# Optimization experiments

Measured on AMD Instinct MI355X. Metric: run time of the kernel, lower is better.

The kernel has to match this reference:

```python
import jax, jax.numpy as jnp
import numpy as np

N_NODES = 100000
N_EDGES = 1200000
N_GRAPHS = 512
IN_DIM, HID, N_CLS = 16, 64, 2
EPS = 1e-5


def setup_inputs() -> dict:
    key = jax.random.key(0)
    ks = jax.random.split(key, 24)
    d = {}
    d["x"] = jax.random.normal(ks[0], (N_NODES, IN_DIM), dtype=jnp.float32)
    d["edge_index"] = jax.random.randint(ks[1], (2, N_EDGES), 0, N_NODES, dtype=jnp.int32)
    d["batch_ids"] = jnp.sort(jax.random.randint(ks[2], (N_NODES,), 0, N_GRAPHS, dtype=jnp.int32))
    # input batchnorm affine
    d["bn_in_g"] = jnp.ones((IN_DIM,), jnp.float32)
    d["bn_in_b"] = jnp.zeros((IN_DIM,), jnp.float32)
    # 3 GCN layers: weight, bias, bn gamma, bn beta
    dims = [(IN_DIM, HID), (HID, HID), (HID, HID)]
    for i, (ci, co) in enumerate(dims):
        s = 1.0 / np.sqrt(ci)
        d[f"W{i}"] = jax.random.uniform(ks[3 + 4 * i], (ci, co), jnp.float32, -s, s)
        d[f"b{i}"] = jnp.zeros((co,), jnp.float32)
        d[f"g{i}"] = jnp.ones((co,), jnp.float32)
        d[f"be{i}"] = jnp.zeros((co,), jnp.float32)
    # classifier head: Linear(HID,HID) -> ReLU -> Linear(HID,N_CLS)
    s = 1.0 / np.sqrt(HID)
    d["Wc1"] = jax.random.uniform(ks[20], (HID, HID), jnp.float32, -s, s)
    d["bc1"] = jax.random.uniform(ks[21], (HID,), jnp.float32, -s, s)
    d["Wc2"] = jax.random.uniform(ks[22], (HID, N_CLS), jnp.float32, -s, s)
    d["bc2"] = jax.random.uniform(ks[23], (N_CLS,), jnp.float32, -s, s)
    return d


def _batchnorm(x, g, b):
    # training-mode BatchNorm1d: biased batch stats over nodes
    m = jnp.mean(x, axis=0)
    v = jnp.mean(jnp.square(x - m), axis=0)
    return (x - m) * jax.lax.rsqrt(v + EPS) * g + b


def _gcn(x, W, b, src, dst, dis):
    # GCNConv: out[i] = sum_{j->i} dis[j]*dis[i] * (x_j W) + b  (self-loops included in src/dst)
    h = x @ W                                  # [N, co]
    msg = h[src] * (dis[src] * dis[dst])[:, None]  # [E+N, co] gather
    return jax.ops.segment_sum(msg, dst, num_segments=N_NODES) + b


def reference(x, bn_in_g, bn_in_b, W0, b0, g0, be0, W1, b1, g1, be1,
              W2, b2, g2, be2, Wc1, bc1, Wc2, bc2, edge_index, batch_ids):
    loops = jnp.arange(N_NODES, dtype=edge_index.dtype)
    src = jnp.concatenate([edge_index[0], loops])
    dst = jnp.concatenate([edge_index[1], loops])
    deg = jax.ops.segment_sum(jnp.ones(src.shape[0], x.dtype), dst, num_segments=N_NODES)
    dis = jnp.where(deg > 0, jax.lax.rsqrt(jnp.maximum(deg, 1e-12)), 0.0)

    h = _batchnorm(x, bn_in_g, bn_in_b)
    for W, b, g, be in ((W0, b0, g0, be0), (W1, b1, g1, be1), (W2, b2, g2, be2)):
        h = jax.nn.relu(_batchnorm(_gcn(h, W, b, src, dst, dis), g, be))

    # global mean pool over graphs
    sums = jax.ops.segment_sum(h, batch_ids, num_segments=N_GRAPHS)
    cnt = jax.ops.segment_sum(jnp.ones((N_NODES,), h.dtype), batch_ids, num_segments=N_GRAPHS)
    pooled = sums / jnp.maximum(cnt, 1.0)[:, None]

    # classifier head (dropout omitted: eval mode)
    z = jax.nn.relu(pooled @ Wc1 + bc1)
    return z @ Wc2 + bc2
```

## Files before the change

kernel.cpp:

```cpp
#include <hip/hip_runtime.h>
#include <hip/hip_bf16.h>

#define N_NODES 100000
#define N_EDGES 1200000
#define N_GRAPHS 512
#define HID 64
#define IN_DIM 16
#define EPS 1e-5f

#define NB_BUCKETS 391
#define BUCKET_SPAN 256
#define REGION 4096
#define BIN_TILE 4096
#define CSR_LEN (N_EDGES + N_NODES)
#define NREP 64


__global__ void bin_kernel(const int* __restrict__ ei, int* __restrict__ bucketCnt,
                           int* __restrict__ regions) {
    __shared__ int hist[NB_BUCKETS], basem[NB_BUCKETS], cur[NB_BUCKETS];
    int t = threadIdx.x;
    for (int i = t; i < NB_BUCKETS; i += 256) { hist[i] = 0; cur[i] = 0; }
    __syncthreads();
    int e0 = blockIdx.x * BIN_TILE;
    int srcs[16], dsts[16];
#pragma unroll
    for (int i = 0; i < 16; i++) {
        int e = e0 + t + i * 256;
        if (e < N_EDGES) {
            srcs[i] = ei[e];
            dsts[i] = ei[N_EDGES + e];
            atomicAdd(&hist[dsts[i] >> 8], 1);
        } else {
            dsts[i] = -1;
        }
    }
    __syncthreads();
    for (int i = t; i < NB_BUCKETS; i += 256) {
        int h = hist[i];
        basem[i] = h ? atomicAdd(&bucketCnt[i], h) : 0;
    }
    __syncthreads();
#pragma unroll
    for (int i = 0; i < 16; i++) {
        if (dsts[i] >= 0) {
            int b = dsts[i] >> 8;
            int pos = basem[b] + atomicAdd(&cur[b], 1);
            if (pos < REGION)
                regions[b * REGION + pos] = srcs[i] | ((dsts[i] & 255) << 17);
        }
    }
}

__global__ void build_kernel(const int* __restrict__ regions, const int* __restrict__ bucketCnt,
                             int* __restrict__ csrOff, int* __restrict__ csrSrc,
                             float* __restrict__ dis) {
    __shared__ int deg[256], off[256], cur[256];
    __shared__ int slice[REGION + 256];
    __shared__ int sTot, sBase;
    int b = blockIdx.x, t = threadIdx.x;
    {
        int s = 0;
        for (int i = t; i < NB_BUCKETS; i += 256)
            if (i < b) s += min(bucketCnt[i], REGION);
        deg[t] = s;
        __syncthreads();
        for (int k = 128; k > 0; k >>= 1) {
            if (t < k) deg[t] += deg[t + k];
            __syncthreads();
        }
        if (t == 0) sBase = deg[0] + b * BUCKET_SPAN;
        __syncthreads();
    }
    int bb = sBase;
    int cnt = min(bucketCnt[b], REGION);
    int nbase = b * BUCKET_SPAN;
    int n = nbase + t;
    bool valid = (n < N_NODES);
    deg[t] = valid ? 1 : 0;
    __syncthreads();
    for (int i = t; i < cnt; i += 256) {
        int rec = regions[b * REGION + i];
        atomicAdd(&deg[rec >> 17], 1);
    }
    __syncthreads();
    int d = deg[t];
    off[t] = d;
    __syncthreads();
    for (int s = 1; s < 256; s <<= 1) {
        int v = (t >= s) ? off[t - s] : 0;
        __syncthreads();
        off[t] += v;
        __syncthreads();
    }
    int excl = off[t] - d;
    if (valid) {
        csrOff[n] = bb + excl;
        dis[n] = rsqrtf((float)d);
    }
    if (b == 0 && t == 0) csrOff[N_NODES] = CSR_LEN;
    if (t == 255) sTot = off[255];
    cur[t] = excl;
    __syncthreads();
    if (valid) {
        int pos = atomicAdd(&cur[t], 1);
        slice[pos] = n;
    }
    for (int i = t; i < cnt; i += 256) {
        int rec = regions[b * REGION + i];
        int pos = atomicAdd(&cur[rec >> 17], 1);
        slice[pos] = rec & 0x1FFFF;
    }
    __syncthreads();
    int tot = sTot;
    for (int i = t; i < tot; i += 256) csrSrc[bb + i] = slice[i];
}


__global__ void stats_x(const float* __restrict__ x, float* __restrict__ sums,
                        float* __restrict__ sumsq, float* __restrict__ hwBuf) {
    __shared__ float ls[16], lq[16];
    int t = threadIdx.x;
    if (blockIdx.x == 0 && t < 16)
        ((float4*)(hwBuf + (size_t)N_NODES * HID))[t] = make_float4(0.f, 0.f, 0.f, 0.f);
    if (t < 16) { ls[t] = 0.f; lq[t] = 0.f; }
    __syncthreads();
    float s = 0.f, q = 0.f;
    const int total = N_NODES * IN_DIM;
    for (int i = blockIdx.x * blockDim.x + t; i < total; i += gridDim.x * blockDim.x) {
        float v = x[i];
        s += v; q += v * v;
    }
    int k = t & 15;
    atomicAdd(&ls[k], s);
    atomicAdd(&lq[k], q);
    __syncthreads();
    if (t < 16) { atomicAdd(&sums[t], ls[t]); atomicAdd(&sumsq[t], lq[t]); }
}

__device__ __forceinline__ void bn_coef(const float* sums, const float* sumsq,
                                        const float* gamma, const float* beta, int k,
                                        float& sc, float& sh) {
    const float invn = 1.0f / (float)N_NODES;
    float m = sums[k] * invn;
    float var = sumsq[k] * invn - m * m;
    float rs = rsqrtf(var + EPS);
    sc = gamma[k] * rs;
    sh = beta[k] - m * sc;
}

__global__ void reduce_stats(const float* __restrict__ rep, float* __restrict__ outStats) {
    int j = threadIdx.x;
    float s = 0.f;
    for (int r = 0; r < NREP; r++) s += rep[r * 128 + j];
    outStats[j] = s;
}


__global__ void premsg_kernel(const float* __restrict__ x, const float* __restrict__ sums,
                              const float* __restrict__ sumsq, const float* __restrict__ gamma,
                              const float* __restrict__ beta, const float* __restrict__ dis,
                              float4* __restrict__ m4) {
    __shared__ float sc16[16], sh16[16];
    int t = threadIdx.x;
    if (t < 16) bn_coef(sums, sumsq, gamma, beta, t, sc16[t], sh16[t]);
    __syncthreads();
    int idx = blockIdx.x * 256 + t;
    if (idx < (N_NODES + 1) * 4) {
        int n = idx >> 2, c = idx & 3;
        float4 v = make_float4(0.f, 0.f, 0.f, 0.f);
        if (n < N_NODES) {
            float4 h = ((const float4*)x)[idx];
            float d = dis[n];
            v.x = (h.x * sc16[c * 4 + 0] + sh16[c * 4 + 0]) * d;
            v.y = (h.y * sc16[c * 4 + 1] + sh16[c * 4 + 1]) * d;
            v.z = (h.z * sc16[c * 4 + 2] + sh16[c * 4 + 2]) * d;
            v.w = (h.w * sc16[c * 4 + 3] + sh16[c * 4 + 3]) * d;
        }
        m4[idx] = v;
    }
}

__global__ void agg16_gemm0_kernel(const float4* __restrict__ m4, const int* __restrict__ csrOff,
                                   const int* __restrict__ csrSrc, const float* __restrict__ dis,
                                   const float* __restrict__ W, const float* __restrict__ bias,
                                   float* __restrict__ y, float* __restrict__ statsRep) {
    __shared__ float Ws[IN_DIM][HID];
    int t = threadIdx.x;
    for (int i = t; i < IN_DIM * HID; i += 256) Ws[i >> 6][i & 63] = W[i];
    __syncthreads();
    const int lane = t & 63;
    const int wid = t >> 6;
    const int q = lane >> 2;
    const int fl = lane & 3;
    const int baseLane = lane & ~3;
    const int wave = blockIdx.x * 4 + wid;
    const int nwaves = gridDim.x * 4;
    float b = bias[lane];
    float sv = 0.f, qv = 0.f;

    for (int n = wave; n < N_NODES; n += nwaves) {
        int beg = csrOff[n], end = csrOff[n + 1];
        float4 acc = make_float4(0.f, 0.f, 0.f, 0.f);
        int e = beg + q;
        int i0 = (e < end) ? csrSrc[e] : N_NODES;
        int i1 = (e + 16 < end) ? csrSrc[e + 16] : N_NODES;
        while (e < end) {
            int j0 = i0, j1 = i1;
            e += 32;
            i0 = (e < end) ? csrSrc[e] : N_NODES;
            i1 = (e + 16 < end) ? csrSrc[e + 16] : N_NODES;
            float4 v0 = m4[(size_t)j0 * 4 + fl];
            float4 v1 = m4[(size_t)j1 * 4 + fl];
            acc.x += v0.x + v1.x; acc.y += v0.y + v1.y;
            acc.z += v0.z + v1.z; acc.w += v0.w + v1.w;
        }
#pragma unroll
        for (int m = 4; m <= 32; m <<= 1) {
            acc.x += __shfl_xor(acc.x, m, 64);
            acc.y += __shfl_xor(acc.y, m, 64);
            acc.z += __shfl_xor(acc.z, m, 64);
            acc.w += __shfl_xor(acc.w, m, 64);
        }
        float d = dis[n];
        acc.x *= d; acc.y *= d; acc.z *= d; acc.w *= d;
        float yv = b;
#pragma unroll
        for (int sf = 0; sf < 4; sf++) {
            float ax = __shfl(acc.x, baseLane + sf, 64);
            float ay = __shfl(acc.y, baseLane + sf, 64);
            float az = __shfl(acc.z, baseLane + sf, 64);
            float aw = __shfl(acc.w, baseLane + sf, 64);
            yv += ax * Ws[sf * 4 + 0][lane];
            yv += ay * Ws[sf * 4 + 1][lane];
            yv += az * Ws[sf * 4 + 2][lane];
            yv += aw * Ws[sf * 4 + 3][lane];
        }
        y[(size_t)n * HID + lane] = yv;
        sv += yv;
        qv += yv * yv;
    }
    __shared__ float ls[4][64], lq[4][64];
    ls[wid][lane] = sv;
    lq[wid][lane] = qv;
    __syncthreads();
    if (wid == 0) {
        float S = ls[0][lane] + ls[1][lane] + ls[2][lane] + ls[3][lane];
        float Q = lq[0][lane] + lq[1][lane] + lq[2][lane] + lq[3][lane];
        float* rep = statsRep + (blockIdx.x & (NREP - 1)) * 128;
        atomicAdd(&rep[lane], S);
        atomicAdd(&rep[64 + lane], Q);
    }
}


#define G64_ROWS 128
__global__ void gemm64_kernel(const float* __restrict__ hin, const float* __restrict__ W,
                              const float* __restrict__ sums, const float* __restrict__ sumsq,
                              const float* __restrict__ gamma, const float* __restrict__ beta,
                              const float* __restrict__ dis, float* __restrict__ hout) {
    __shared__ float Ws[HID * HID];
    __shared__ float hs[G64_ROWS][HID + 1];
    __shared__ float scb[64], shb[64];
    int t = threadIdx.x;
    int fg = t & 15;
    int rg = t >> 4;
    int base = blockIdx.x * G64_ROWS;

    if (t < 64) bn_coef(sums, sumsq, gamma, beta, t, scb[t], shb[t]);
    {
        const float4* W4 = (const float4*)W;
        float4* Ws4 = (float4*)Ws;
        for (int i = t; i < HID * HID / 4; i += 256) Ws4[i] = W4[i];
    }
    __syncthreads();
    {
        const float4* hin4 = (const float4*)hin;
        for (int i = t; i < G64_ROWS * 16; i += 256) {
            int r = i >> 4, c = i & 15;
            int n = base + r;
            float4 v = make_float4(0.f, 0.f, 0.f, 0.f);
            if (n < N_NODES) {
                float4 h = hin4[n * 16 + c];
                v.x = fmaxf(h.x * scb[c * 4 + 0] + shb[c * 4 + 0], 0.f);
                v.y = fmaxf(h.y * scb[c * 4 + 1] + shb[c * 4 + 1], 0.f);
                v.z = fmaxf(h.z * scb[c * 4 + 2] + shb[c * 4 + 2], 0.f);
                v.w = fmaxf(h.w * scb[c * 4 + 3] + shb[c * 4 + 3], 0.f);
            }
            hs[r][c * 4 + 0] = v.x;
            hs[r][c * 4 + 1] = v.y;
            hs[r][c * 4 + 2] = v.z;
            hs[r][c * 4 + 3] = v.w;
        }
    }
    __syncthreads();

    float4 acc[8];
#pragma unroll
    for (int r = 0; r < 8; r++) acc[r] = make_float4(0.f, 0.f, 0.f, 0.f);
    const float4* Ws4 = (const float4*)Ws;
    for (int k = 0; k < HID; k++) {
        float4 wk = Ws4[k * 16 + fg];
#pragma unroll
        for (int r = 0; r < 8; r++) {
            float h = hs[rg * 8 + r][k];
            acc[r].x += h * wk.x;
            acc[r].y += h * wk.y;
            acc[r].z += h * wk.z;
            acc[r].w += h * wk.w;
        }
    }
    float4* hout4 = (float4*)hout;
#pragma unroll
    for (int r = 0; r < 8; r++) {
        int n = base + rg * 8 + r;
        if (n < N_NODES) {
            float dsc = dis[n];
            float4 o = acc[r];
            o.x *= dsc; o.y *= dsc; o.z *= dsc; o.w *= dsc;
            hout4[n * 16 + fg] = o;
        }
    }
}


__global__ void aggregate_kernel(const float4* __restrict__ hw4, const int* __restrict__ csrOff,
                                 const int* __restrict__ csrSrc, const float* __restrict__ dis,
                                 const float* __restrict__ bias, float4* __restrict__ y4,
                                 float* __restrict__ statsRep) {
    const int lane = threadIdx.x & 63;
    const int wid = threadIdx.x >> 6;
    const int q = lane >> 4;
    const int fl = lane & 15;
    const int wave = blockIdx.x * 4 + wid;
    const int nwaves = gridDim.x * 4;

    const float4 bias4 = ((const float4*)bias)[fl];
    float4 s_acc = make_float4(0.f, 0.f, 0.f, 0.f);
    float4 q_acc = make_float4(0.f, 0.f, 0.f, 0.f);

    for (int n = wave; n < N_NODES; n += nwaves) {
        int beg = csrOff[n], end = csrOff[n + 1];
        float4 acc = make_float4(0.f, 0.f, 0.f, 0.f);
        int e = beg + q;
        int i0 = (e < end) ? csrSrc[e] : N_NODES;
        int i1 = (e + 4 < end) ? csrSrc[e + 4] : N_NODES;
        while (e < end) {
            int j0 = i0, j1 = i1;
            e += 8;
            i0 = (e < end) ? csrSrc[e] : N_NODES;
            i1 = (e + 4 < end) ? csrSrc[e + 4] : N_NODES;
            float4 v0 = hw4[(size_t)j0 * 16 + fl];
            float4 v1 = hw4[(size_t)j1 * 16 + fl];
            acc.x += v0.x + v1.x; acc.y += v0.y + v1.y;
            acc.z += v0.z + v1.z; acc.w += v0.w + v1.w;
        }
        acc.x += __shfl_xor(acc.x, 16, 64);
        acc.y += __shfl_xor(acc.y, 16, 64);
        acc.z += __shfl_xor(acc.z, 16, 64);
        acc.w += __shfl_xor(acc.w, 16, 64);
        acc.x += __shfl_xor(acc.x, 32, 64);
        acc.y += __shfl_xor(acc.y, 32, 64);
        acc.z += __shfl_xor(acc.z, 32, 64);
        acc.w += __shfl_xor(acc.w, 32, 64);
        if (q == 0) {
            float d = dis[n];
            float4 val;
            val.x = acc.x * d + bias4.x;
            val.y = acc.y * d + bias4.y;
            val.z = acc.z * d + bias4.z;
            val.w = acc.w * d + bias4.w;
            y4[(size_t)n * 16 + fl] = val;
            s_acc.x += val.x; s_acc.y += val.y; s_acc.z += val.z; s_acc.w += val.w;
            q_acc.x += val.x * val.x; q_acc.y += val.y * val.y;
            q_acc.z += val.z * val.z; q_acc.w += val.w * val.w;
        }
    }
    __shared__ float ls[4][64], lq[4][64];
    ls[wid][lane] = 0.f;
    lq[wid][lane] = 0.f;
    if (q == 0) {
        ls[wid][fl * 4 + 0] = s_acc.x; ls[wid][fl * 4 + 1] = s_acc.y;
        ls[wid][fl * 4 + 2] = s_acc.z; ls[wid][fl * 4 + 3] = s_acc.w;
        lq[wid][fl * 4 + 0] = q_acc.x; lq[wid][fl * 4 + 1] = q_acc.y;
        lq[wid][fl * 4 + 2] = q_acc.z; lq[wid][fl * 4 + 3] = q_acc.w;
    }
    __syncthreads();
    if (wid == 0) {
        float S = ls[0][lane] + ls[1][lane] + ls[2][lane] + ls[3][lane];
        float Q = lq[0][lane] + lq[1][lane] + lq[2][lane] + lq[3][lane];
        float* rep = statsRep + (blockIdx.x & (NREP - 1)) * 128;
        atomicAdd(&rep[lane], S);
        atomicAdd(&rep[64 + lane], Q);
    }
}


#define POOL_CHUNK 256
__global__ void pool_kernel(const float* __restrict__ y, const int* __restrict__ batch,
                            const float* __restrict__ sums, const float* __restrict__ sumsq,
                            const float* __restrict__ gamma, const float* __restrict__ beta,
                            float* __restrict__ pool, float* __restrict__ cnt) {
    int f = threadIdx.x & 63;
    int nl = threadIdx.x >> 6;
    float sc, sh;
    bn_coef(sums, sumsq, gamma, beta, f, sc, sh);
    int base = blockIdx.x * POOL_CHUNK;
    int endn = min(base + POOL_CHUNK, N_NODES);
    int g_cur = -1;
    float acc = 0.f;
    float c_acc = 0.f;
    for (int n = base + nl; n < endn; n += 4) {
        int g = batch[n];
        float v = fmaxf(y[n * HID + f] * sc + sh, 0.f);
        if (g != g_cur) {
            if (g_cur >= 0) {
                atomicAdd(&pool[g_cur * HID + f], acc);
                if (f == 0) atomicAdd(&cnt[g_cur], c_acc);
            }
            g_cur = g;
            acc = 0.f;
            c_acc = 0.f;
        }
        acc += v;
        c_acc += 1.f;
    }
    if (g_cur >= 0) {
        atomicAdd(&pool[g_cur * HID + f], acc);
        if (f == 0) atomicAdd(&cnt[g_cur], c_acc);
    }
}

__global__ void head_kernel(const float* __restrict__ pool, const float* __restrict__ cnt,
                            const float* __restrict__ Wc1, const float* __restrict__ bc1,
                            const float* __restrict__ Wc2, const float* __restrict__ bc2,
                            float* __restrict__ out) {
    int g = blockIdx.x;
    int f = threadIdx.x;
    __shared__ float p[64], z[64];
    float c = fmaxf(cnt[g], 1.0f);
    p[f] = pool[g * HID + f] / c;
    __syncthreads();
    float acc = bc1[f];
    for (int k = 0; k < 64; k++) acc += p[k] * Wc1[k * 64 + f];
    z[f] = fmaxf(acc, 0.f);
    __syncthreads();
    if (f < 2) {
        float o = bc2[f];
        for (int k = 0; k < 64; k++) o += z[k] * Wc2[k * 2 + f];
        out[g * 2 + f] = o;
    }
}


extern "C" void kernel_launch(void* const* d_in, const int* in_sizes, int n_in,
                              void* d_out, int out_size, void* d_ws, size_t ws_size,
                              hipStream_t stream) {
    const float* x      = (const float*)d_in[0];
    const int*   ei     = (const int*)d_in[1];
    const int*   batch  = (const int*)d_in[2];
    const float* bn_in_g = (const float*)d_in[3];
    const float* bn_in_b = (const float*)d_in[4];
    const float* W0 = (const float*)d_in[5];
    const float* b0 = (const float*)d_in[6];
    const float* g0 = (const float*)d_in[7];
    const float* be0 = (const float*)d_in[8];
    const float* W1 = (const float*)d_in[9];
    const float* b1 = (const float*)d_in[10];
    const float* g1 = (const float*)d_in[11];
    const float* be1 = (const float*)d_in[12];
    const float* W2 = (const float*)d_in[13];
    const float* b2 = (const float*)d_in[14];
    const float* g2 = (const float*)d_in[15];
    const float* be2 = (const float*)d_in[16];
    const float* Wc1 = (const float*)d_in[17];
    const float* bc1 = (const float*)d_in[18];
    const float* Wc2 = (const float*)d_in[19];
    const float* bc2 = (const float*)d_in[20];
    float* out = (float*)d_out;

    char* w = (char*)d_ws;
    size_t off = 0;
    auto take = [&](size_t bytes) {
        size_t r = off;
        off += (bytes + 255) & ~(size_t)255;
        return r;
    };
    float* stats    = (float*)(w + take(4 * 256 * 4));
    float* statsRep = (float*)(w + take(3 * NREP * 128 * 4));
    float* pool     = (float*)(w + take((size_t)N_GRAPHS * HID * 4));
    float* cnt      = (float*)(w + take((size_t)N_GRAPHS * 4));
    int* bucketCnt  = (int*)(w + take((size_t)NB_BUCKETS * 4));
    size_t zero_end = off;
    float* dis    = (float*)(w + take((size_t)N_NODES * 4));
    int* csrOff   = (int*)(w + take((size_t)(N_NODES + 1) * 4));
    int* csrSrc   = (int*)(w + take((size_t)(CSR_LEN + 64) * 4));
    float* hwBuf  = (float*)(w + take((size_t)(N_NODES + 1) * HID * 4));
    float* yBuf   = (float*)(w + take((size_t)N_NODES * HID * 4));
    int* regions  = (int*)hwBuf;
    float* msgBuf = (float*)hwBuf;
    (void)ws_size; (void)n_in; (void)in_sizes; (void)out_size;

    hipMemsetAsync(w, 0, zero_end, stream);

    const int nbBin  = (N_EDGES + BIN_TILE - 1) / BIN_TILE;
    const int nbPre  = ((N_NODES + 1) * 4 + 255) / 256;
    const int nbG64  = (N_NODES + G64_ROWS - 1) / G64_ROWS;
    const int nbAgg  = 4096;

    bin_kernel<<<nbBin, 256, 0, stream>>>(ei, bucketCnt, regions);
    build_kernel<<<NB_BUCKETS, 256, 0, stream>>>(regions, bucketCnt, csrOff, csrSrc, dis);

    float* s0 = stats + 0 * 256;
    float* s1 = stats + 1 * 256;
    float* s2 = stats + 2 * 256;
    float* s3 = stats + 3 * 256;
    float* rep1 = statsRep + 0 * NREP * 128;
    float* rep2 = statsRep + 1 * NREP * 128;
    float* rep3 = statsRep + 2 * NREP * 128;

    stats_x<<<256, 256, 0, stream>>>(x, s0, s0 + 64, hwBuf);

    premsg_kernel<<<nbPre, 256, 0, stream>>>(x, s0, s0 + 64, bn_in_g, bn_in_b, dis,
                                             (float4*)msgBuf);
    agg16_gemm0_kernel<<<nbAgg, 256, 0, stream>>>((const float4*)msgBuf, csrOff, csrSrc, dis,
                                                  W0, b0, yBuf, rep1);
    reduce_stats<<<1, 128, 0, stream>>>(rep1, s1);

    gemm64_kernel<<<nbG64, 256, 0, stream>>>(yBuf, W1, s1, s1 + 64, g0, be0, dis, hwBuf);
    aggregate_kernel<<<nbAgg, 256, 0, stream>>>((const float4*)hwBuf, csrOff, csrSrc, dis, b1,
                                                (float4*)yBuf, rep2);
    reduce_stats<<<1, 128, 0, stream>>>(rep2, s2);

    gemm64_kernel<<<nbG64, 256, 0, stream>>>(yBuf, W2, s2, s2 + 64, g1, be1, dis, hwBuf);
    aggregate_kernel<<<nbAgg, 256, 0, stream>>>((const float4*)hwBuf, csrOff, csrSrc, dis, b2,
                                                (float4*)yBuf, rep3);
    reduce_stats<<<1, 128, 0, stream>>>(rep3, s3);

    const int nbPool = (N_NODES + POOL_CHUNK - 1) / POOL_CHUNK;
    pool_kernel<<<nbPool, 256, 0, stream>>>(yBuf, batch, s3, s3 + 64, g2, be2, pool, cnt);
    head_kernel<<<N_GRAPHS, 64, 0, stream>>>(pool, cnt, Wc1, bc1, Wc2, bc2, out);
}
```

Before: 367.8 us.

## Store gathered message buffers in fp16 and widen aggregation lanes to half8

The pre-scaled message buffers that the aggregation kernels gather from are now stored as fp16 instead of fp32, which halves the bytes moved per random neighbor gather. The 64-wide aggregation is remapped so each lane loads a half8 (16 bytes), letting 8 edges be processed in parallel per wave instead of 4, with accumulation still done in fp32. The 16-dim message buffer gets its own allocation rather than aliasing hwBuf. The cost is reduced precision in the messages, which may perturb the batchnorm statistics and the final outputs.

```diff
diff --git a/kernel.cpp b/kernel.cpp
--- a/kernel.cpp
+++ b/kernel.cpp
@@ -14,6 +14,9 @@
 #define BIN_TILE 4096
 #define CSR_LEN (N_EDGES + N_NODES)
 #define NREP 64
+
+typedef _Float16 half4 __attribute__((ext_vector_type(4)));
+typedef _Float16 half8 __attribute__((ext_vector_type(8)));
 
 
 __global__ void bin_kernel(const int* __restrict__ ei, int* __restrict__ bucketCnt,
@@ -118,10 +121,10 @@
 
 
 __global__ void stats_x(const float* __restrict__ x, float* __restrict__ sums,
-                        float* __restrict__ sumsq, float* __restrict__ hwBuf) {
+                        float* __restrict__ sumsq, _Float16* __restrict__ hwBuf) {
     __shared__ float ls[16], lq[16];
     int t = threadIdx.x;
-    if (blockIdx.x == 0 && t < 16)
+    if (blockIdx.x == 0 && t < 8)
         ((float4*)(hwBuf + (size_t)N_NODES * HID))[t] = make_float4(0.f, 0.f, 0.f, 0.f);
     if (t < 16) { ls[t] = 0.f; lq[t] = 0.f; }
     __syncthreads();
@@ -160,7 +163,7 @@
 __global__ void premsg_kernel(const float* __restrict__ x, const float* __restrict__ sums,
                               const float* __restrict__ sumsq, const float* __restrict__ gamma,
                               const float* __restrict__ beta, const float* __restrict__ dis,
-                              float4* __restrict__ m4) {
+                              half4* __restrict__ m4) {
     __shared__ float sc16[16], sh16[16];
     int t = threadIdx.x;
     if (t < 16) bn_coef(sums, sumsq, gamma, beta, t, sc16[t], sh16[t]);
@@ -168,20 +171,21 @@
     int idx = blockIdx.x * 256 + t;
     if (idx < (N_NODES + 1) * 4) {
         int n = idx >> 2, c = idx & 3;
-        float4 v = make_float4(0.f, 0.f, 0.f, 0.f);
+        half4 o;
+        o.x = (_Float16)0.f; o.y = (_Float16)0.f; o.z = (_Float16)0.f; o.w = (_Float16)0.f;
         if (n < N_NODES) {
             float4 h = ((const float4*)x)[idx];
             float d = dis[n];
-            v.x = (h.x * sc16[c * 4 + 0] + sh16[c * 4 + 0]) * d;
-            v.y = (h.y * sc16[c * 4 + 1] + sh16[c * 4 + 1]) * d;
-            v.z = (h.z * sc16[c * 4 + 2] + sh16[c * 4 + 2]) * d;
-            v.w = (h.w * sc16[c * 4 + 3] + sh16[c * 4 + 3]) * d;
-        }
-        m4[idx] = v;
-    }
-}
-
-__global__ void agg16_gemm0_kernel(const float4* __restrict__ m4, const int* __restrict__ csrOff,
+            o.x = (_Float16)((h.x * sc16[c * 4 + 0] + sh16[c * 4 + 0]) * d);
+            o.y = (_Float16)((h.y * sc16[c * 4 + 1] + sh16[c * 4 + 1]) * d);
+            o.z = (_Float16)((h.z * sc16[c * 4 + 2] + sh16[c * 4 + 2]) * d);
+            o.w = (_Float16)((h.w * sc16[c * 4 + 3] + sh16[c * 4 + 3]) * d);
+        }
+        m4[idx] = o;
+    }
+}
+
+__global__ void agg16_gemm0_kernel(const half4* __restrict__ m4, const int* __restrict__ csrOff,
                                    const int* __restrict__ csrSrc, const float* __restrict__ dis,
                                    const float* __restrict__ W, const float* __restrict__ bias,
                                    float* __restrict__ y, float* __restrict__ statsRep) {
@@ -210,10 +214,12 @@
             e += 32;
             i0 = (e < end) ? csrSrc[e] : N_NODES;
             i1 = (e + 16 < end) ? csrSrc[e + 16] : N_NODES;
-            float4 v0 = m4[(size_t)j0 * 4 + fl];
-            float4 v1 = m4[(size_t)j1 * 4 + fl];
-            acc.x += v0.x + v1.x; acc.y += v0.y + v1.y;
-            acc.z += v0.z + v1.z; acc.w += v0.w + v1.w;
+            half4 v0 = m4[(size_t)j0 * 4 + fl];
+            half4 v1 = m4[(size_t)j1 * 4 + fl];
+            acc.x += (float)v0.x + (float)v1.x;
+            acc.y += (float)v0.y + (float)v1.y;
+            acc.z += (float)v0.z + (float)v1.z;
+            acc.w += (float)v0.w + (float)v1.w;
         }
 #pragma unroll
         for (int m = 4; m <= 32; m <<= 1) {
@@ -258,7 +264,7 @@
 __global__ void gemm64_kernel(const float* __restrict__ hin, const float* __restrict__ W,
                               const float* __restrict__ sums, const float* __restrict__ sumsq,
                               const float* __restrict__ gamma, const float* __restrict__ beta,
-                              const float* __restrict__ dis, float* __restrict__ hout) {
+                              const float* __restrict__ dis, _Float16* __restrict__ hout) {
     __shared__ float Ws[HID * HID];
     __shared__ float hs[G64_ROWS][HID + 1];
     __shared__ float scb[64], shb[64];
@@ -310,80 +316,83 @@
             acc[r].w += h * wk.w;
         }
     }
-    float4* hout4 = (float4*)hout;
+    half4* hout4 = (half4*)hout;
 #pragma unroll
     for (int r = 0; r < 8; r++) {
         int n = base + rg * 8 + r;
         if (n < N_NODES) {
             float dsc = dis[n];
-            float4 o = acc[r];
-            o.x *= dsc; o.y *= dsc; o.z *= dsc; o.w *= dsc;
+            half4 o;
+            o.x = (_Float16)(acc[r].x * dsc);
+            o.y = (_Float16)(acc[r].y * dsc);
+            o.z = (_Float16)(acc[r].z * dsc);
+            o.w = (_Float16)(acc[r].w * dsc);
             hout4[n * 16 + fg] = o;
         }
     }
 }
 
 
-__global__ void aggregate_kernel(const float4* __restrict__ hw4, const int* __restrict__ csrOff,
+__global__ void aggregate_kernel(const half8* __restrict__ hwh, const int* __restrict__ csrOff,
                                  const int* __restrict__ csrSrc, const float* __restrict__ dis,
                                  const float* __restrict__ bias, float4* __restrict__ y4,
                                  float* __restrict__ statsRep) {
     const int lane = threadIdx.x & 63;
     const int wid = threadIdx.x >> 6;
-    const int q = lane >> 4;
-    const int fl = lane & 15;
+    const int o = lane >> 3;
+    const int c = lane & 7;
     const int wave = blockIdx.x * 4 + wid;
     const int nwaves = gridDim.x * 4;
 
-    const float4 bias4 = ((const float4*)bias)[fl];
-    float4 s_acc = make_float4(0.f, 0.f, 0.f, 0.f);
-    float4 q_acc = make_float4(0.f, 0.f, 0.f, 0.f);
+    const float4 bv0 = ((const float4*)bias)[c * 2];
+    const float4 bv1 = ((const float4*)bias)[c * 2 + 1];
+    float sa[8], qa[8];
+#pragma unroll
+    for (int j = 0; j < 8; j++) { sa[j] = 0.f; qa[j] = 0.f; }
 
     for (int n = wave; n < N_NODES; n += nwaves) {
         int beg = csrOff[n], end = csrOff[n + 1];
-        float4 acc = make_float4(0.f, 0.f, 0.f, 0.f);
-        int e = beg + q;
+        float acc[8];
+#pragma unroll
+        for (int j = 0; j < 8; j++) acc[j] = 0.f;
+        int e = beg + o;
         int i0 = (e < end) ? csrSrc[e] : N_NODES;
-        int i1 = (e + 4 < end) ? csrSrc[e + 4] : N_NODES;
+        int i1 = (e + 8 < end) ? csrSrc[e + 8] : N_NODES;
         while (e < end) {
             int j0 = i0, j1 = i1;
-            e += 8;
+            e += 16;
             i0 = (e < end) ? csrSrc[e] : N_NODES;
-            i1 = (e + 4 < end) ? csrSrc[e + 4] : N_NODES;
-            float4 v0 = hw4[(size_t)j0 * 16 + fl];
-            float4 v1 = hw4[(size_t)j1 * 16 + fl];
-            acc.x += v0.x + v1.x; acc.y += v0.y + v1.y;
-            acc.z += v0.z + v1.z; acc.w += v0.w + v1.w;
-        }
-        acc.x += __shfl_xor(acc.x, 16, 64);
-        acc.y += __shfl_xor(acc.y, 16, 64);
-        acc.z += __shfl_xor(acc.z, 16, 64);
-        acc.w += __shfl_xor(acc.w, 16, 64);
-        acc.x += __shfl_xor(acc.x, 32, 64);
-        acc.y += __shfl_xor(acc.y, 32, 64);
-        acc.z += __shfl_xor(acc.z, 32, 64);
-        acc.w += __shfl_xor(acc.w, 32, 64);
-        if (q == 0) {
+            i1 = (e + 8 < end) ? csrSrc[e + 8] : N_NODES;
+            half8 h0 = hwh[(size_t)j0 * 8 + c];
+            half8 h1 = hwh[(size_t)j1 * 8 + c];
+#pragma unroll
+            for (int j = 0; j < 8; j++) acc[j] += (float)h0[j] + (float)h1[j];
+        }
+#pragma unroll
+        for (int j = 0; j < 8; j++) {
+            acc[j] += __shfl_xor(acc[j], 8, 64);
+            acc[j] += __shfl_xor(acc[j], 16, 64);
+            acc[j] += __shfl_xor(acc[j], 32, 64);
+        }
+        if (o == 0) {
             float d = dis[n];
-            float4 val;
-            val.x = acc.x * d + bias4.x;
-            val.y = acc.y * d + bias4.y;
-            val.z = acc.z * d + bias4.z;
-            val.w = acc.w * d + bias4.w;
-            y4[(size_t)n * 16 + fl] = val;
-            s_acc.x += val.x; s_acc.y += val.y; s_acc.z += val.z; s_acc.w += val.w;
-            q_acc.x += val.x * val.x; q_acc.y += val.y * val.y;
-            q_acc.z += val.z * val.z; q_acc.w += val.w * val.w;
+            float val[8];
+            val[0] = acc[0] * d + bv0.x; val[1] = acc[1] * d + bv0.y;
+            val[2] = acc[2] * d + bv0.z; val[3] = acc[3] * d + bv0.w;
+            val[4] = acc[4] * d + bv1.x; val[5] = acc[5] * d + bv1.y;
+            val[6] = acc[6] * d + bv1.z; val[7] = acc[7] * d + bv1.w;
+            y4[(size_t)n * 16 + c * 2] = make_float4(val[0], val[1], val[2], val[3]);
+            y4[(size_t)n * 16 + c * 2 + 1] = make_float4(val[4], val[5], val[6], val[7]);
+#pragma unroll
+            for (int j = 0; j < 8; j++) { sa[j] += val[j]; qa[j] += val[j] * val[j]; }
         }
     }
     __shared__ float ls[4][64], lq[4][64];
     ls[wid][lane] = 0.f;
     lq[wid][lane] = 0.f;
-    if (q == 0) {
-        ls[wid][fl * 4 + 0] = s_acc.x; ls[wid][fl * 4 + 1] = s_acc.y;
-        ls[wid][fl * 4 + 2] = s_acc.z; ls[wid][fl * 4 + 3] = s_acc.w;
-        lq[wid][fl * 4 + 0] = q_acc.x; lq[wid][fl * 4 + 1] = q_acc.y;
-        lq[wid][fl * 4 + 2] = q_acc.z; lq[wid][fl * 4 + 3] = q_acc.w;
+    if (o == 0) {
+#pragma unroll
+        for (int j = 0; j < 8; j++) { ls[wid][c * 8 + j] = sa[j]; lq[wid][c * 8 + j] = qa[j]; }
     }
     __syncthreads();
     if (wid == 0) {
@@ -495,10 +504,10 @@
     float* dis    = (float*)(w + take((size_t)N_NODES * 4));
     int* csrOff   = (int*)(w + take((size_t)(N_NODES + 1) * 4));
     int* csrSrc   = (int*)(w + take((size_t)(CSR_LEN + 64) * 4));
-    float* hwBuf  = (float*)(w + take((size_t)(N_NODES + 1) * HID * 4));
+    _Float16* hwBuf = (_Float16*)(w + take((size_t)(N_NODES + 1) * HID * 2));
     float* yBuf   = (float*)(w + take((size_t)N_NODES * HID * 4));
+    _Float16* msgBuf = (_Float16*)(w + take((size_t)(N_NODES + 1) * IN_DIM * 2));
     int* regions  = (int*)hwBuf;
-    float* msgBuf = (float*)hwBuf;
     (void)ws_size; (void)n_in; (void)in_sizes; (void)out_size;
 
     hipMemsetAsync(w, 0, zero_end, stream);
@@ -522,18 +531,18 @@
     stats_x<<<256, 256, 0, stream>>>(x, s0, s0 + 64, hwBuf);
 
     premsg_kernel<<<nbPre, 256, 0, stream>>>(x, s0, s0 + 64, bn_in_g, bn_in_b, dis,
-                                             (float4*)msgBuf);
-    agg16_gemm0_kernel<<<nbAgg, 256, 0, stream>>>((const float4*)msgBuf, csrOff, csrSrc, dis,
+                                             (half4*)msgBuf);
+    agg16_gemm0_kernel<<<nbAgg, 256, 0, stream>>>((const half4*)msgBuf, csrOff, csrSrc, dis,
                                                   W0, b0, yBuf, rep1);
     reduce_stats<<<1, 128, 0, stream>>>(rep1, s1);
 
     gemm64_kernel<<<nbG64, 256, 0, stream>>>(yBuf, W1, s1, s1 + 64, g0, be0, dis, hwBuf);
-    aggregate_kernel<<<nbAgg, 256, 0, stream>>>((const float4*)hwBuf, csrOff, csrSrc, dis, b1,
+    aggregate_kernel<<<nbAgg, 256, 0, stream>>>((const half8*)hwBuf, csrOff, csrSrc, dis, b1,
                                                 (float4*)yBuf, rep2);
     reduce_stats<<<1, 128, 0, stream>>>(rep2, s2);
 
     gemm64_kernel<<<nbG64, 256, 0, stream>>>(yBuf, W2, s2, s2 + 64, g1, be1, dis, hwBuf);
-    aggregate_kernel<<<nbAgg, 256, 0, stream>>>((const float4*)hwBuf, csrOff, csrSrc, dis, b2,
+    aggregate_kernel<<<nbAgg, 256, 0, stream>>>((const half8*)hwBuf, csrOff, csrSrc, dis, b2,
                                                 (float4*)yBuf, rep3);
     reduce_stats<<<1, 128, 0, stream>>>(rep3, s3);
 
```

Result: faster. 344.7 us (-6.3%).
